# Optimization experiments

Measured on AMD Instinct MI355X. Metric: run time of the kernel, lower is better.

Reference implementation:

```python
import jax, jax.numpy as jnp
import numpy as np

DIM = 1024
N_HEADS = 16
DIM_FF = 4096
EPS = 1e-12


def layer_norm(x, gamma, beta):
    u = jnp.mean(x, axis=-1, keepdims=True)
    s = jnp.mean((x - u) ** 2, axis=-1, keepdims=True)
    return gamma * ((x - u) / jnp.sqrt(s + EPS)) + beta


def setup_inputs() -> dict:
    key = jax.random.key(0)
    ks = jax.random.split(key, 12)
    B, S, D, F = 2, 2048, DIM, DIM_FF
    init = lambda k, shape: (jax.random.normal(k, shape, dtype=jnp.float32) * 0.02)
    return {
        "x": jax.random.normal(ks[0], (B, S, D), dtype=jnp.float32),
        "mask": jnp.ones((B, S), dtype=jnp.int32),
        "wq": init(ks[1], (D, D)), "bq": jnp.zeros((D,), jnp.float32),
        "wk": init(ks[2], (D, D)), "bk": jnp.zeros((D,), jnp.float32),
        "wv": init(ks[3], (D, D)), "bv": jnp.zeros((D,), jnp.float32),
        "wo": init(ks[4], (D, D)), "bo": jnp.zeros((D,), jnp.float32),
        "g1": jnp.ones((D,), jnp.float32), "b1": jnp.zeros((D,), jnp.float32),
        "w1": init(ks[5], (D, F)), "bf1": jnp.zeros((F,), jnp.float32),
        "w2": init(ks[6], (F, D)), "bf2": jnp.zeros((D,), jnp.float32),
        "g2": jnp.ones((D,), jnp.float32), "b2": jnp.zeros((D,), jnp.float32),
    }


def reference(x, mask, wq, bq, wk, bk, wv, bv, wo, bo, g1, b1, w1, bf1, w2, bf2, g2, b2):
    B, S, D = x.shape
    H = N_HEADS
    W = D // H
    # QKV projections -> (B, H, S, W)
    def heads(y):
        return y.reshape(B, S, H, W).transpose(0, 2, 1, 3)
    q = heads(x @ wq + bq)
    k = heads(x @ wk + bk)
    v = heads(x @ wv + bv)
    # scaled dot-product attention with additive mask (exact module math)
    scores = jnp.einsum('bhsw,bhtw->bhst', q, k) / np.sqrt(W).astype(np.float32)
    m = mask.astype(jnp.float32)[:, None, None, :]  # (B,1,1,S)
    scores = scores - 10000.0 * (1.0 - m)
    attn = jax.nn.softmax(scores, axis=-1)
    h = jnp.einsum('bhst,bhtw->bhsw', attn, v).transpose(0, 2, 1, 3).reshape(B, S, D)
    # residual + LN1
    h = layer_norm(x + (h @ wo + bo), g1, b1)
    # position-wise FFN with exact-erf GELU, residual + LN2
    ff = jax.nn.gelu(h @ w1 + bf1, approximate=False) @ w2 + bf2
    return layer_norm(h + ff, g2, b2)
```

## Files before the change

### kernel.cpp

```cpp
#include <hip/hip_runtime.h>
#include <cstdint>
#include <cstddef>

using u16 = unsigned short;
using u32 = unsigned int;
using u64 = unsigned long long;

typedef __bf16 bf16x8 __attribute__((ext_vector_type(8)));
typedef float f32x4 __attribute__((ext_vector_type(4)));

static constexpr int Bb = 2, S = 2048, D = 1024, H = 16, W = 64, F = 4096;
static constexpr int M = Bb * S;

__device__ __forceinline__ float bf2f(u16 u) {
  union { u32 i; float f; } c; c.i = ((u32)u) << 16; return c.f;
}
__device__ __forceinline__ u16 f2bf(float f) {
  union { float f; u32 i; } c; c.f = f;
  u32 i = c.i;
  u32 r = (i + 0x7fffu + ((i >> 16) & 1u)) >> 16;
  return (u16)r;
}
__device__ __forceinline__ u16 f2bf_cvt(float f) {
  __bf16 b = (__bf16)f;
  union { __bf16 b; u16 u; } c; c.b = b; return c.u;
}
__device__ __forceinline__ __bf16 u2b(u16 x) {
  union { u16 u; __bf16 b; } c; c.u = x; return c.b;
}
__device__ __forceinline__ void stv(float* p, size_t i, float v) { p[i] = v; }
__device__ __forceinline__ void stv(u16* p, size_t i, float v)   { p[i] = f2bf(v); }
__device__ __forceinline__ float ldv(const float* p, size_t i) { return p[i]; }
__device__ __forceinline__ float ldv(const u16* p, size_t i)   { return bf2f(p[i]); }

__device__ __forceinline__ void async_cp16(const u16* g, u16* l) {
  __builtin_amdgcn_global_load_lds(
      (const __attribute__((address_space(1))) void*)g,
      (__attribute__((address_space(3))) void*)l, 16, 0, 0);
}

__device__ __forceinline__ void swizzle8(int& bx, int& by) {
  int bid = blockIdx.y * gridDim.x + blockIdx.x;
  int gpr = gridDim.x >> 3;
  int grp = bid >> 6, rem = bid & 63;
  int gm = grp / gpr, gn = grp - gm * gpr;
  by = gm * 8 + (rem >> 3);
  bx = gn * 8 + (rem & 7);
}

__global__ __launch_bounds__(256) void conv_x_kernel(
    const float* __restrict__ src, u16* __restrict__ dst)
{
  int i = (blockIdx.x * 256 + threadIdx.x) * 4;
  float4 v = *(const float4*)(src + i);
  u16 r[4] = { f2bf(v.x), f2bf(v.y), f2bf(v.z), f2bf(v.w) };
  *(uint2*)(dst + i) = *(const uint2*)r;
}

__global__ __launch_bounds__(256) void transpose_w_kernel(
    const float* __restrict__ src, u16* __restrict__ dst, int K, int N)
{
  __shared__ __align__(16) u16 T[64][72];
  const int tid = threadIdx.x;
  const int n0 = blockIdx.x * 64, k0 = blockIdx.y * 64;
#pragma unroll
  for (int t = 0; t < 4; t++) {
    int idx = tid + t * 256;
    int r = idx >> 4, c4 = (idx & 15) * 4;
    float4 v = *(const float4*)(src + (size_t)(k0 + r) * N + n0 + c4);
    T[c4 + 0][r] = f2bf(v.x); T[c4 + 1][r] = f2bf(v.y);
    T[c4 + 2][r] = f2bf(v.z); T[c4 + 3][r] = f2bf(v.w);
  }
  __syncthreads();
#pragma unroll
  for (int t = 0; t < 2; t++) {
    int idx = tid + t * 256;
    int r = idx >> 3, c8 = (idx & 7) * 8;
    *(uint4*)(dst + (size_t)(n0 + r) * K + k0 + c8) = *(const uint4*)(&T[r][c8]);
  }
}

template<int EPI, typename TC>
__global__ __launch_bounds__(256) void gemm_bt(
    const u16* __restrict__ A, const u16* __restrict__ BT,
    const float* __restrict__ bias, TC* __restrict__ C,
    int N, int K, float scale)
{
  __shared__ __align__(16) u16 As[2][128 * 32];
  __shared__ __align__(16) u16 Bs[2][128 * 32];
  const int tid = threadIdx.x;
  const int wave = tid >> 6, lane = tid & 63;
  const int quad = lane >> 4, l16 = lane & 15;
  int bx, by; swizzle8(bx, by);
  const int m0 = by * 128, n0 = bx * 128;
  const int wm = (wave >> 1) * 64, wn = (wave & 1) * 64;
  const int srow = lane >> 2;
  const int skoff = (lane & 3) * 8;

  f32x4 acc[4][4] = {};

  for (int k0 = 0; k0 < K; k0 += 64) {
#pragma unroll
    for (int h = 0; h < 2; h++) {
#pragma unroll
      for (int t = 0; t < 2; t++) {
        int slot = wave * 2 + t;
        int row = slot * 16 + srow;
        const u16* ga = A  + (size_t)(m0 + row) * K + k0 + h * 32 + skoff;
        const u16* gb = BT + (size_t)(n0 + row) * K + k0 + h * 32 + skoff;
        async_cp16(ga, As[h] + slot * 512);
        async_cp16(gb, Bs[h] + slot * 512);
      }
    }
    __syncthreads();

#pragma unroll
    for (int h = 0; h < 2; h++) {
      bf16x8 af[4], bfv[4];
#pragma unroll
      for (int i = 0; i < 4; i++)
        af[i] = *(const bf16x8*)(As[h] + (wm + i * 16 + l16) * 32 + quad * 8);
#pragma unroll
      for (int j = 0; j < 4; j++)
        bfv[j] = *(const bf16x8*)(Bs[h] + (wn + j * 16 + l16) * 32 + quad * 8);
#pragma unroll
      for (int i = 0; i < 4; i++)
#pragma unroll
        for (int j = 0; j < 4; j++)
          acc[i][j] = __builtin_amdgcn_mfma_f32_16x16x32_bf16(af[i], bfv[j], acc[i][j], 0, 0, 0);
    }
    __syncthreads();
  }

#pragma unroll
  for (int i = 0; i < 4; i++) {
#pragma unroll
    for (int j = 0; j < 4; j++) {
#pragma unroll
      for (int r = 0; r < 4; r++) {
        int row = m0 + wm + i * 16 + quad * 4 + r;
        int col = n0 + wn + j * 16 + l16;
        float val = acc[i][j][r] + bias[col];
        if (EPI == 1) {
          val = 0.5f * val * (1.0f + erff(val * 0.70710678118654752f));
        }
        if (EPI == 2) {
          int sel = col >> 10, c = col & 1023;
          if (sel == 0) val *= scale;
          int bb = row >> 11, ss = row & 2047;
          int hh = c >> 6,  ww = c & 63;
          u16* dst = (u16*)C + (size_t)sel * M * D;
          dst[(((size_t)(bb * H + hh) * S) + ss) * W + ww] = f2bf(val);
        } else {
          stv(C, (size_t)row * N + col, val);
        }
      }
    }
  }
}

template<typename TC>
__global__ __launch_bounds__(256) void gemm_bt_n64(
    const u16* __restrict__ A, const u16* __restrict__ BT,
    const float* __restrict__ bias, TC* __restrict__ C,
    int N, int K)
{
  __shared__ __align__(16) u16 As[2][128 * 32];
  __shared__ __align__(16) u16 Bs[2][64 * 32];
  const int tid = threadIdx.x;
  const int wave = tid >> 6, lane = tid & 63;
  const int quad = lane >> 4, l16 = lane & 15;
  int bx, by; swizzle8(bx, by);
  const int m0 = by * 128, n0 = bx * 64;
  const int wm = (wave >> 1) * 64, wn = (wave & 1) * 32;
  const int srow = lane >> 2;
  const int skoff = (lane & 3) * 8;

  f32x4 acc[4][2] = {};

  for (int k0 = 0; k0 < K; k0 += 64) {
#pragma unroll
    for (int h = 0; h < 2; h++) {
#pragma unroll
      for (int t = 0; t < 2; t++) {
        int slot = wave * 2 + t;
        int row = slot * 16 + srow;
        async_cp16(A + (size_t)(m0 + row) * K + k0 + h * 32 + skoff, As[h] + slot * 512);
      }
      int row = wave * 16 + srow;
      async_cp16(BT + (size_t)(n0 + row) * K + k0 + h * 32 + skoff, Bs[h] + wave * 512);
    }
    __syncthreads();

#pragma unroll
    for (int h = 0; h < 2; h++) {
      bf16x8 af[4], bfv[2];
#pragma unroll
      for (int i = 0; i < 4; i++)
        af[i] = *(const bf16x8*)(As[h] + (wm + i * 16 + l16) * 32 + quad * 8);
#pragma unroll
      for (int j = 0; j < 2; j++)
        bfv[j] = *(const bf16x8*)(Bs[h] + (wn + j * 16 + l16) * 32 + quad * 8);
#pragma unroll
      for (int i = 0; i < 4; i++)
#pragma unroll
        for (int j = 0; j < 2; j++)
          acc[i][j] = __builtin_amdgcn_mfma_f32_16x16x32_bf16(af[i], bfv[j], acc[i][j], 0, 0, 0);
    }
    __syncthreads();
  }

#pragma unroll
  for (int i = 0; i < 4; i++) {
#pragma unroll
    for (int j = 0; j < 2; j++) {
#pragma unroll
      for (int r = 0; r < 4; r++) {
        int row = m0 + wm + i * 16 + quad * 4 + r;
        int col = n0 + wn + j * 16 + l16;
        stv(C, (size_t)row * N + col, acc[i][j][r] + bias[col]);
      }
    }
  }
}

__global__ __launch_bounds__(256) void transpose_v_kernel(
    const u16* __restrict__ v, u16* __restrict__ vt)
{
  __shared__ __align__(16) u16 T[64][72];
  const int bh = blockIdx.y, k0 = blockIdx.x * 64, tid = threadIdx.x;
#pragma unroll
  for (int it = 0; it < 2; it++) {
    int vv = tid + it * 256;
    int key = vv >> 3, w0 = (vv & 7) * 8;
    union { uint4 q; u16 e[8]; } u;
    u.q = *(const uint4*)(v + ((size_t)bh * S + k0 + key) * W + w0);
#pragma unroll
    for (int j = 0; j < 8; j++) T[w0 + j][key] = u.e[j];
  }
  __syncthreads();
#pragma unroll
  for (int it = 0; it < 2; it++) {
    int vv = tid + it * 256;
    int w = vv >> 3, koff = (vv & 7) * 8;
    *(uint4*)(vt + ((size_t)bh * W + w) * S + k0 + koff) = *(const uint4*)(&T[w][koff]);
  }
}

__global__ __launch_bounds__(256) void fattn_kernel(
    const u16* __restrict__ q, const u16* __restrict__ k,
    const u16* __restrict__ vt, const int* __restrict__ mask,
    u16* __restrict__ o_parts, float* __restrict__ l_parts)
{
  __shared__ __align__(16) u16 QP[2][128][32];
  __shared__ __align__(16) u16 Kl[2][64][32];
  __shared__ __align__(16) u16 Vl[2][64][32];

  const int tid = threadIdx.x, wave = tid >> 6, lane = tid & 63;
  const int quad = lane >> 4, l16 = lane & 15;
  const int bh = blockIdx.y, b = bh >> 4, h = bh & 15;
  const int q0 = blockIdx.x * 128;
  const int half = blockIdx.z;
  const int kbase = half * (S / 2);
  const int wq0 = wave * 32;
  const int sr  = tid >> 3;
  const int sg  = tid & 7;
  const int sp  = sg >> 2;
  const int sc0 = sg * 8;
  const int ssw = (((sg & 3) ^ ((sr >> 1) & 3)) << 3);
  const int xr = (l16 >> 1) & 3;
  const int rq = ((quad ^ xr) << 3);

#pragma unroll
  for (int t = 0; t < 4; t++) {
    int row = sr + t * 32;
    *(uint4*)(&QP[sp][row][ssw]) =
        *(const uint4*)(q + ((size_t)bh * S + q0 + row) * W + sc0);
  }
  __syncthreads();
  bf16x8 aq[2][2];
#pragma unroll
  for (int g = 0; g < 2; g++)
#pragma unroll
    for (int kc = 0; kc < 2; kc++)
      aq[g][kc] = *(const bf16x8*)(&QP[kc][wq0 + g * 16 + l16][rq]);

  bf16x8 ones;
  {
    u16 ov = (l16 == 0) ? (u16)0x3F80 : (u16)0;
#pragma unroll
    for (int j = 0; j < 8; j++) ones[j] = u2b(ov);
  }

  f32x4 o_acc[2][4] = {};
  f32x4 l_acc[2] = {};

  uint4 kr0, kr1, vr0, vr1;
  int mv;
  kr0 = *(const uint4*)(k  + ((size_t)bh * S + kbase + sr     ) * W + sc0);
  kr1 = *(const uint4*)(k  + ((size_t)bh * S + kbase + sr + 32) * W + sc0);
  vr0 = *(const uint4*)(vt + ((size_t)bh * W + sr     ) * S + kbase + sc0);
  vr1 = *(const uint4*)(vt + ((size_t)bh * W + sr + 32) * S + kbase + sc0);
  mv  = mask[b * S + kbase + lane];

  constexpr int NT = S / 128;
  for (int kt = 0; kt < NT; kt++) {
    __syncthreads();
    *(uint4*)(&Kl[sp][sr     ][ssw]) = kr0;
    *(uint4*)(&Kl[sp][sr + 32][ssw]) = kr1;
    *(uint4*)(&Vl[sp][sr     ][ssw]) = vr0;
    *(uint4*)(&Vl[sp][sr + 32][ssw]) = vr1;
    u64 km = __ballot(mv != 0);
    __syncthreads();

    if (kt + 1 < NT) {
      int kn = kbase + (kt + 1) * 64;
      kr0 = *(const uint4*)(k  + ((size_t)bh * S + kn + sr     ) * W + sc0);
      kr1 = *(const uint4*)(k  + ((size_t)bh * S + kn + sr + 32) * W + sc0);
      vr0 = *(const uint4*)(vt + ((size_t)bh * W + sr     ) * S + kn + sc0);
      vr1 = *(const uint4*)(vt + ((size_t)bh * W + sr + 32) * S + kn + sc0);
      mv  = mask[b * S + kn + lane];
    }

#pragma unroll
    for (int tn = 0; tn < 4; tn++) {
      bf16x8 bk0 = *(const bf16x8*)(&Kl[0][tn * 16 + l16][rq]);
      bf16x8 bk1 = *(const bf16x8*)(&Kl[1][tn * 16 + l16][rq]);
      u32 nib = (u32)(km >> (tn * 16 + quad * 4)) & 0xFu;
      int slotp = (((tn & 1) * 2 + (quad >> 1)) ^ xr) * 8 + (quad & 1) * 4;
#pragma unroll
      for (int g = 0; g < 2; g++) {
        f32x4 s4 = {};
        s4 = __builtin_amdgcn_mfma_f32_16x16x32_bf16(bk0, aq[g][0], s4, 0, 0, 0);
        s4 = __builtin_amdgcn_mfma_f32_16x16x32_bf16(bk1, aq[g][1], s4, 0, 0, 0);
        union { u64 u; u16 e[4]; } pw;
#pragma unroll
        for (int r = 0; r < 4; r++) {
          float pm = (float)((nib >> r) & 1u);
          pw.e[r] = f2bf_cvt(__expf(s4[r]) * pm);
        }
        *(u64*)(&QP[tn >> 1][wq0 + g * 16 + l16][slotp]) = pw.u;
      }
    }

#pragma unroll
    for (int kc = 0; kc < 2; kc++) {
      bf16x8 ap0 = *(const bf16x8*)(&QP[kc][wq0      + l16][rq]);
      bf16x8 ap1 = *(const bf16x8*)(&QP[kc][wq0 + 16 + l16][rq]);
#pragma unroll
      for (int tn = 0; tn < 4; tn++) {
        bf16x8 bv = *(const bf16x8*)(&Vl[kc][tn * 16 + l16][rq]);
        o_acc[0][tn] = __builtin_amdgcn_mfma_f32_16x16x32_bf16(ap0, bv, o_acc[0][tn], 0, 0, 0);
        o_acc[1][tn] = __builtin_amdgcn_mfma_f32_16x16x32_bf16(ap1, bv, o_acc[1][tn], 0, 0, 0);
      }
      l_acc[0] = __builtin_amdgcn_mfma_f32_16x16x32_bf16(ap0, ones, l_acc[0], 0, 0, 0);
      l_acc[1] = __builtin_amdgcn_mfma_f32_16x16x32_bf16(ap1, ones, l_acc[1], 0, 0, 0);
    }
  }

  u16* ob = o_parts + (size_t)half * M * D;
  float* lb = l_parts + (size_t)half * M * H;
#pragma unroll
  for (int g = 0; g < 2; g++) {
#pragma unroll
    for (int r = 0; r < 4; r++) {
      float lsum = __shfl(l_acc[g][r], lane & 0x30);
      int sg2 = q0 + wq0 + g * 16 + quad * 4 + r;
      if (l16 == 0) lb[((size_t)b * S + sg2) * H + h] = lsum;
#pragma unroll
      for (int tn = 0; tn < 4; tn++) {
        ob[((size_t)b * S + sg2) * D + h * W + tn * 16 + l16] = f2bf_cvt(o_acc[g][tn][r]);
      }
    }
  }
}

__global__ __launch_bounds__(256) void combine_attn(
    const u16* __restrict__ o_parts, const float* __restrict__ l_parts,
    u16* __restrict__ attn)
{
  size_t idx = ((size_t)blockIdx.x * 256 + threadIdx.x) * 8;
  int row = (int)(idx >> 10);
  int h = ((int)idx >> 6) & 15;
  float l = l_parts[(size_t)row * H + h] + l_parts[(size_t)M * H + (size_t)row * H + h];
  float inv = 1.0f / l;
  union { uint4 v; u16 e[8]; } a, bq, o;
  a.v  = *(const uint4*)(o_parts + idx);
  bq.v = *(const uint4*)(o_parts + (size_t)M * D + idx);
#pragma unroll
  for (int j = 0; j < 8; j++)
    o.e[j] = f2bf((bf2f(a.e[j]) + bf2f(bq.e[j])) * inv);
  *(uint4*)(attn + idx) = o.v;
}

template<typename TA, typename TR, typename TO>
__global__ __launch_bounds__(256) void ln_res_kernel(
    const TA* __restrict__ a, const TR* __restrict__ r,
    const float* __restrict__ g, const float* __restrict__ be,
    TO* __restrict__ out)
{
  const int tid = threadIdx.x, lane = tid & 63;
  const int row = blockIdx.x * 4 + (tid >> 6);
  const TA* ap = a + (size_t)row * D;
  const TR* rp = r + (size_t)row * D;
  float hv[16];
  float s = 0.f;
#pragma unroll
  for (int c = 0; c < 16; c++) {
    int d = c * 64 + lane;
    hv[c] = ldv(ap, d) + ldv(rp, d);
    s += hv[c];
  }
#pragma unroll
  for (int d = 1; d < 64; d <<= 1) s += __shfl_xor(s, d);
  float mean = s * (1.0f / D);
  float v = 0.f;
#pragma unroll
  for (int c = 0; c < 16; c++) { float t = hv[c] - mean; v += t * t; }
#pragma unroll
  for (int d = 1; d < 64; d <<= 1) v += __shfl_xor(v, d);
  float inv = rsqrtf(v * (1.0f / D) + 1e-12f);
#pragma unroll
  for (int c = 0; c < 16; c++) {
    int d = c * 64 + lane;
    stv(out, (size_t)row * D + d, g[d] * ((hv[c] - mean) * inv) + be[d]);
  }
}

extern "C" void kernel_launch(void* const* d_in, const int* in_sizes, int n_in,
                              void* d_out, int out_size, void* d_ws, size_t ws_size,
                              hipStream_t stream)
{
  const float* x  = (const float*)d_in[0];
  const int* mask = (const int*)d_in[1];
  const float* wq = (const float*)d_in[2];  const float* bq  = (const float*)d_in[3];
  const float* wk = (const float*)d_in[4];  const float* bk  = (const float*)d_in[5];
  const float* wv = (const float*)d_in[6];  const float* bv  = (const float*)d_in[7];
  const float* wo = (const float*)d_in[8];  const float* bo  = (const float*)d_in[9];
  const float* g1 = (const float*)d_in[10]; const float* b1  = (const float*)d_in[11];
  const float* w1 = (const float*)d_in[12]; const float* bf1 = (const float*)d_in[13];
  const float* w2 = (const float*)d_in[14]; const float* bf2 = (const float*)d_in[15];
  const float* g2 = (const float*)d_in[16]; const float* b2  = (const float*)d_in[17];

  char* ws = (char*)d_ws;
  const size_t MB = 1024 * 1024;
  u16* wqkvT = (u16*)(ws + 0 * MB);
  u16* woT   = (u16*)(ws + 6 * MB);
  u16* w1T   = (u16*)(ws + 0 * MB);
  u16* w2T   = (u16*)(ws + 0 * MB);
  u16* xb    = (u16*)(ws + 8 * MB);
  u16* vt    = (u16*)(ws + 8 * MB);
  u16* q     = (u16*)(ws + 16 * MB);
  u16* proj  = (u16*)(ws + 16 * MB);
  u16* kb    = (u16*)(ws + 24 * MB);
  u16* vb    = (u16*)(ws + 32 * MB);
  u16* oparts = (u16*)(ws + 32 * MB);
  float* lparts = (float*)(ws + 0 * MB);
  u16* attn  = (u16*)(ws + 32 * MB);
  u16* ff1   = (u16*)(ws + 8 * MB);
  float* bqkv = (float*)(ws + 40 * MB);
  u16* h1    = (u16*)(ws + 40 * MB);
  float* out = (float*)d_out;

  dim3 blk(256);

  conv_x_kernel<<<dim3(M * D / 1024), blk, 0, stream>>>(x, xb);
  transpose_w_kernel<<<dim3(16, 16), blk, 0, stream>>>(wq, wqkvT,            D, D);
  transpose_w_kernel<<<dim3(16, 16), blk, 0, stream>>>(wk, wqkvT + 1024*1024, D, D);
  transpose_w_kernel<<<dim3(16, 16), blk, 0, stream>>>(wv, wqkvT + 2048*1024, D, D);
  transpose_w_kernel<<<dim3(16, 16), blk, 0, stream>>>(wo, woT,              D, D);
  hipMemcpyAsync(bqkv,        bq, D * sizeof(float), hipMemcpyDeviceToDevice, stream);
  hipMemcpyAsync(bqkv + 1024, bk, D * sizeof(float), hipMemcpyDeviceToDevice, stream);
  hipMemcpyAsync(bqkv + 2048, bv, D * sizeof(float), hipMemcpyDeviceToDevice, stream);

  gemm_bt<2, u16><<<dim3(3072 / 128, M / 128), blk, 0, stream>>>(
      xb, wqkvT, bqkv, q, 3072, D, 0.125f);

  transpose_v_kernel<<<dim3(S / 64, Bb * H), blk, 0, stream>>>(vb, vt);
  fattn_kernel<<<dim3(S / 128, Bb * H, 2), blk, 0, stream>>>(
      q, kb, vt, mask, oparts, lparts);
  combine_attn<<<dim3(M * D / 2048), blk, 0, stream>>>(oparts, lparts, attn);

  gemm_bt_n64<u16><<<dim3(D / 64, M / 128), blk, 0, stream>>>(
      attn, woT, bo, proj, D, D);
  ln_res_kernel<float, u16, u16><<<dim3(M / 4), blk, 0, stream>>>(x, proj, g1, b1, h1);

  transpose_w_kernel<<<dim3(F / 64, D / 64), blk, 0, stream>>>(w1, w1T, D, F);
  gemm_bt<1, u16><<<dim3(F / 128, M / 128), blk, 0, stream>>>(
      h1, w1T, bf1, ff1, F, D, 1.0f);

  transpose_w_kernel<<<dim3(D / 64, F / 64), blk, 0, stream>>>(w2, w2T, F, D);
  gemm_bt_n64<float><<<dim3(D / 64, M / 128), blk, 0, stream>>>(
      ff1, w2T, bf2, out, D, F);
  ln_res_kernel<u16, float, float><<<dim3(M / 4), blk, 0, stream>>>(h1, out, g2, b2, out);
}
```

Measured before the change: 416.4 us.

## Add 256x256-tile 8-wave GEMM with fused GELU for FFN up-projection

Replaces the 128x128 gemm_bt used for h1@w1 with a new 256x256-tile kernel running 512 threads (8 waves). It uses XOR-swizzled LDS, async global-to-LDS copies, double buffering, interleaved loads and MFMA phases, and s_setprio around the MFMA blocks. The larger tile is meant to raise operand reuse and MFMA utilisation on the largest GEMM. In exchange it launches only 256 blocks and needs heavy register and LDS use per block, which may limit occupancy. The GELU epilogue is removed from the generic gemm_bt template, so it now lives only in the new kernel.

```diff
diff --git a/kernel.cpp b/kernel.cpp
--- a/kernel.cpp
+++ b/kernel.cpp
@@ -141,9 +141,6 @@
         int row = m0 + wm + i * 16 + quad * 4 + r;
         int col = n0 + wn + j * 16 + l16;
         float val = acc[i][j][r] + bias[col];
-        if (EPI == 1) {
-          val = 0.5f * val * (1.0f + erff(val * 0.70710678118654752f));
-        }
         if (EPI == 2) {
           int sel = col >> 10, c = col & 1023;
           if (sel == 0) val *= scale;
@@ -154,6 +151,153 @@
         } else {
           stv(C, (size_t)row * N + col, val);
         }
+      }
+    }
+  }
+}
+
+__global__ __launch_bounds__(512, 2) void gemm256_gelu(
+    const u16* __restrict__ A, const u16* __restrict__ BT,
+    const float* __restrict__ bias, u16* __restrict__ C)
+{
+  constexpr int GN = F, GK = D, NT = GK / 64;
+  __shared__ __align__(16) u16 AL[2][2][128 * 64];
+  __shared__ __align__(16) u16 BL[2][2][128 * 64];
+  const int tid = threadIdx.x;
+  const int wave = tid >> 6, lane = tid & 63;
+  const int quad = lane >> 4, l16 = lane & 15;
+  const int wm = wave >> 2, wn = wave & 3;
+  int bx, by; swizzle8(bx, by);
+  const int m0 = by * 256, n0 = bx * 256;
+  const int lr = lane >> 3;
+  const int kc8 = ((lane & 7) ^ lr) * 8;
+  const int xb = (l16 & 7) * 16;
+  const int brow0 = (wn & 1) * 64;
+  const char* abase = (const char*)&AL[0][wm][0];
+  const char* bbase = (const char*)&BL[0][wn >> 1][0];
+  constexpr int BUFB = 2 * 128 * 64 * 2;
+
+  f32x4 acc[8][4] = {};
+
+  auto stA = [&](int t, int buf) {
+#pragma unroll
+    for (int half = 0; half < 2; half++)
+#pragma unroll
+      for (int j = 0; j < 2; j++) {
+        const u16* g = A + (size_t)(m0 + half * 128 + (j * 8 + wave) * 8 + lr) * GK
+                         + t * 64 + kc8;
+        async_cp16(g, &AL[buf][half][(j * 8 + wave) * 512]);
+      }
+  };
+  auto stB = [&](int t, int buf, int half) {
+#pragma unroll
+    for (int j = 0; j < 2; j++) {
+      const u16* g = BT + (size_t)(n0 + half * 128 + (j * 8 + wave) * 8 + lr) * GK
+                        + t * 64 + kc8;
+      async_cp16(g, &BL[buf][half][(j * 8 + wave) * 512]);
+    }
+  };
+
+  stA(0, 0);
+  stB(0, 0, 0); stB(0, 0, 1);
+  stB(1, 1, 0); stB(1, 1, 1);
+  asm volatile("s_waitcnt vmcnt(4)" ::: "memory");
+  __builtin_amdgcn_s_barrier();
+
+  bf16x8 af[4][2], bf0[2][2], bf1v[2][2];
+
+#pragma unroll 2
+  for (int t = 0; t < NT; t++) {
+    const int buf = t & 1;
+    const char* ab = abase + buf * BUFB;
+    const char* bb = bbase + buf * BUFB;
+
+#pragma unroll
+    for (int i = 0; i < 4; i++)
+#pragma unroll
+      for (int s = 0; s < 2; s++)
+        af[i][s] = *(const bf16x8*)(ab + (i * 16 + l16) * 128 + (((s * 4 + quad) * 16) ^ xb));
+#pragma unroll
+    for (int j = 0; j < 2; j++)
+#pragma unroll
+      for (int s = 0; s < 2; s++)
+        bf0[j][s] = *(const bf16x8*)(bb + (brow0 + j * 16 + l16) * 128 + (((s * 4 + quad) * 16) ^ xb));
+    stA((t + 1) & (NT - 1), buf ^ 1);
+    __builtin_amdgcn_s_barrier();
+    __builtin_amdgcn_s_setprio(1);
+#pragma unroll
+    for (int i = 0; i < 4; i++)
+#pragma unroll
+      for (int j = 0; j < 2; j++)
+#pragma unroll
+        for (int s = 0; s < 2; s++)
+          acc[i][j] = __builtin_amdgcn_mfma_f32_16x16x32_bf16(af[i][s], bf0[j][s], acc[i][j], 0, 0, 0);
+    __builtin_amdgcn_s_setprio(0);
+    __builtin_amdgcn_s_barrier();
+
+#pragma unroll
+    for (int j = 0; j < 2; j++)
+#pragma unroll
+      for (int s = 0; s < 2; s++)
+        bf1v[j][s] = *(const bf16x8*)(bb + (brow0 + 32 + j * 16 + l16) * 128 + (((s * 4 + quad) * 16) ^ xb));
+    __builtin_amdgcn_s_barrier();
+    __builtin_amdgcn_s_setprio(1);
+#pragma unroll
+    for (int i = 0; i < 4; i++)
+#pragma unroll
+      for (int j = 0; j < 2; j++)
+#pragma unroll
+        for (int s = 0; s < 2; s++)
+          acc[i][2 + j] = __builtin_amdgcn_mfma_f32_16x16x32_bf16(af[i][s], bf1v[j][s], acc[i][2 + j], 0, 0, 0);
+    __builtin_amdgcn_s_setprio(0);
+    __builtin_amdgcn_s_barrier();
+
+#pragma unroll
+    for (int i = 0; i < 4; i++)
+#pragma unroll
+      for (int s = 0; s < 2; s++)
+        af[i][s] = *(const bf16x8*)(ab + (64 + i * 16 + l16) * 128 + (((s * 4 + quad) * 16) ^ xb));
+    stB((t + 2) & (NT - 1), buf, 0);
+    __builtin_amdgcn_s_barrier();
+    __builtin_amdgcn_s_setprio(1);
+#pragma unroll
+    for (int i = 0; i < 4; i++)
+#pragma unroll
+      for (int j = 0; j < 2; j++)
+#pragma unroll
+        for (int s = 0; s < 2; s++)
+          acc[4 + i][2 + j] = __builtin_amdgcn_mfma_f32_16x16x32_bf16(af[i][s], bf1v[j][s], acc[4 + i][2 + j], 0, 0, 0);
+    __builtin_amdgcn_s_setprio(0);
+    __builtin_amdgcn_s_barrier();
+
+    stB((t + 2) & (NT - 1), buf, 1);
+    __builtin_amdgcn_s_barrier();
+    __builtin_amdgcn_s_setprio(1);
+#pragma unroll
+    for (int i = 0; i < 4; i++)
+#pragma unroll
+      for (int j = 0; j < 2; j++)
+#pragma unroll
+        for (int s = 0; s < 2; s++)
+          acc[4 + i][j] = __builtin_amdgcn_mfma_f32_16x16x32_bf16(af[i][s], bf0[j][s], acc[4 + i][j], 0, 0, 0);
+    __builtin_amdgcn_s_setprio(0);
+    asm volatile("s_waitcnt vmcnt(4)" ::: "memory");
+    __builtin_amdgcn_s_barrier();
+  }
+
+  asm volatile("s_waitcnt vmcnt(0)" ::: "memory");
+
+#pragma unroll
+  for (int i = 0; i < 8; i++) {
+#pragma unroll
+    for (int j = 0; j < 4; j++) {
+#pragma unroll
+      for (int r = 0; r < 4; r++) {
+        int row = m0 + wm * 128 + i * 16 + quad * 4 + r;
+        int col = n0 + wn * 64 + j * 16 + l16;
+        float val = acc[i][j][r] + bias[col];
+        val = 0.5f * val * (1.0f + erff(val * 0.70710678118654752f));
+        C[(size_t)row * GN + col] = f2bf(val);
       }
     }
   }
@@ -486,8 +630,8 @@
   ln_res_kernel<float, u16, u16><<<dim3(M / 4), blk, 0, stream>>>(x, proj, g1, b1, h1);
 
   transpose_w_kernel<<<dim3(F / 64, D / 64), blk, 0, stream>>>(w1, w1T, D, F);
-  gemm_bt<1, u16><<<dim3(F / 128, M / 128), blk, 0, stream>>>(
-      h1, w1T, bf1, ff1, F, D, 1.0f);
+  gemm256_gelu<<<dim3(F / 256, M / 256), dim3(512), 0, stream>>>(
+      h1, w1T, bf1, ff1);
 
   transpose_w_kernel<<<dim3(D / 64, F / 64), blk, 0, stream>>>(w2, w2T, F, D);
   gemm_bt_n64<float><<<dim3(D / 64, M / 128), blk, 0, stream>>>(
```

After: 401.9 us. -3.5%, faster.
